# Optimization experiments

Hardware: AMD Instinct MI355X
Metric: run time of the kernel (lower is better)

Reference implementation:

```python
import jax, jax.numpy as jnp
import numpy as np

N_NODES = 50000
N_EDGES = 800000
IN_CH, HID_CH, OUT_CH = 128, 128, 40


def _glorot(key, fan_in, fan_out):
    lim = jnp.sqrt(6.0 / (fan_in + fan_out))
    return jax.random.uniform(key, (fan_in, fan_out), jnp.float32, -lim, lim)


def setup_inputs() -> dict:
    key = jax.random.key(0)
    ks = jax.random.split(key, 5)
    x = jax.random.normal(ks[0], (N_NODES, IN_CH), jnp.float32)
    edge_index = jax.random.randint(ks[1], (2, N_EDGES), 0, N_NODES, dtype=jnp.int32)
    return {
        "x": x,
        "edge_index": edge_index,
        "W1": _glorot(ks[2], IN_CH, HID_CH),
        "b1": jnp.zeros((HID_CH,), jnp.float32),
        "W2": _glorot(ks[3], HID_CH, HID_CH),
        "b2": jnp.zeros((HID_CH,), jnp.float32),
        "W3": _glorot(ks[4], HID_CH, OUT_CH),
        "b3": jnp.zeros((OUT_CH,), jnp.float32),
    }


def reference(x, edge_index, W1, b1, W2, b2, W3, b3):
    # Dropout is inference-mode identity (training=False). GCNConv (PyG default):
    # add self-loops, symmetric normalization D^-1/2 A_hat D^-1/2, linear + bias.
    n = x.shape[0]
    loop = jnp.arange(n, dtype=edge_index.dtype)
    src = jnp.concatenate([edge_index[0], loop])  # message sources
    dst = jnp.concatenate([edge_index[1], loop])  # aggregation targets
    deg = jax.ops.segment_sum(jnp.ones_like(src, dtype=x.dtype), dst, num_segments=n)
    dinv = jnp.where(deg > 0, deg ** -0.5, 0.0)
    norm = dinv[src] * dinv[dst]  # [E+N], identical across layers

    def conv(h, W, b):
        h = h @ W                                   # [N, F_out]
        msg = h[src] * norm[:, None]                # gather + scale: [E+N, F_out]
        return jax.ops.segment_sum(msg, dst, num_segments=n) + b

    h = jax.nn.relu(conv(x, W1, b1))
    h = jax.nn.relu(conv(h, W2, b2))
    h = conv(h, W3, b3)
    return jax.nn.log_softmax(h, axis=1)
```

## Files before the change

kernel.cpp:

```cpp
#include <hip/hip_runtime.h>
#include <math.h>


typedef short s8v __attribute__((ext_vector_type(8)));
typedef float f4v __attribute__((ext_vector_type(4)));
typedef unsigned short u16;

#define CSR_CAP 64

__device__ inline unsigned short f2b(float f) {
  unsigned int u = __float_as_uint(f);
  return (unsigned short)((u + 0x7fffu + ((u >> 16) & 1u)) >> 16);
}
__device__ inline float b2f(unsigned short b) {
  return __uint_as_float(((unsigned int)b) << 16);
}
__device__ inline f4v mfma16(s8v a, s8v b, f4v c) {
  return __builtin_amdgcn_mfma_f32_16x16x32_bf16(a, b, c, 0, 0, 0);
}

__device__ inline void pack_w_elem(const float* __restrict__ W,
                                   short* __restrict__ Wp, int FOUT_real,
                                   int NCT, int idx) {
  const int j = idx & 7;
  const int lane = (idx >> 3) & 63;
  const int fct = idx >> 9;
  const int ks = fct / NCT, ct = fct - ks * NCT;
  const int k = ks * 32 + (lane >> 4) * 8 + j;
  const int c = ct * 16 + (lane & 15);
  const float v = (c < FOUT_real) ? W[k * FOUT_real + c] : 0.f;
  Wp[idx] = (short)f2b(v);
}

__global__ __launch_bounds__(256) void k_soup(
    const float* __restrict__ x, const float* __restrict__ W1,
    short* __restrict__ Tb1, int nRowTiles, int gemmNB,
    const int* __restrict__ src, const int* __restrict__ dst,
    int* __restrict__ cnt, u16* __restrict__ col, int e, float inv8n,
    int fillNB, const float* __restrict__ W2, short* __restrict__ Wp2,
    const float* __restrict__ W3, short* __restrict__ Wp3) {
  __shared__ short Ws[4 * 8 * 64 * 8];
  const int bid = blockIdx.x;
  const int tid = threadIdx.x;

  if (bid < gemmNB) {
    const float4* w4 = (const float4*)W1;
    for (int it = 0; it < 16; ++it) {
      const int lin4 = it * 256 + tid;
      const int k = lin4 >> 5;
      const float4 v = w4[lin4];
      const int cb = (lin4 & 31) * 4;
      const int ks = k >> 5, kr = k & 31;
      const int laneBase = (kr >> 3) << 4;
      const int j = kr & 7;
      const float fv[4] = {v.x, v.y, v.z, v.w};
#pragma unroll
      for (int q = 0; q < 4; ++q) {
        const int c = cb + q;
        Ws[((ks * 8 + (c >> 4)) * 64 + (laneBase | (c & 15))) * 8 + j] =
            (short)f2b(fv[q]);
      }
    }
    __syncthreads();
    const int wid = tid >> 6, lane = tid & 63;
    const int rowTile = bid * 4 + wid;
    if (rowTile >= nRowTiles) return;
    const int row0 = rowTile * 16;
    const int arow = row0 + (lane & 15);
    const int kcol = (lane >> 4) * 8;
    f4v acc[8];
#pragma unroll
    for (int ct = 0; ct < 8; ++ct) acc[ct] = (f4v)(0.f);
    const float* ap = x + (size_t)arow * 128 + kcol;
#pragma unroll
    for (int ks = 0; ks < 4; ++ks) {
      const float4 a0 = *(const float4*)(ap + ks * 32);
      const float4 a1 = *(const float4*)(ap + ks * 32 + 4);
      s8v af;
      af[0] = (short)f2b(a0.x); af[1] = (short)f2b(a0.y);
      af[2] = (short)f2b(a0.z); af[3] = (short)f2b(a0.w);
      af[4] = (short)f2b(a1.x); af[5] = (short)f2b(a1.y);
      af[6] = (short)f2b(a1.z); af[7] = (short)f2b(a1.w);
#pragma unroll
      for (int ct = 0; ct < 8; ++ct) {
        const s8v bf = *(const s8v*)(Ws + ((ks * 8 + ct) * 64 + lane) * 8);
        acc[ct] = mfma16(af, bf, acc[ct]);
      }
    }
    const int crow0 = row0 + (lane >> 4) * 4;
    const int ccol = lane & 15;
#pragma unroll
    for (int r = 0; r < 4; ++r) {
      short* orow = Tb1 + (size_t)(crow0 + r) * 128 + ccol;
#pragma unroll
      for (int ct = 0; ct < 8; ++ct) orow[ct * 16] = (short)f2b(acc[ct][r]);
    }
  } else if (bid < gemmNB + fillNB) {
    const int fb = bid - gemmNB;
    const int bin = fb & 7;
    const int scanB = fb >> 3;
    const int stride = (fillNB >> 3) * 256;
    for (int i = scanB * 256 + tid; i < e; i += stride) {
      const int d = dst[i];
      int b = (int)((float)d * inv8n);
      b = b > 7 ? 7 : b;
      if (b == bin) {
        const int idx = atomicAdd(&cnt[d], 1);
        __builtin_nontemporal_store((u16)src[i], &col[(size_t)d * CSR_CAP + idx]);
      }
    }
  } else {
    int pb = bid - gemmNB - fillNB;
    if (pb < 64) {
      pack_w_elem(W2, Wp2, 128, 8, pb * 256 + tid);
    } else {
      const int idx = (pb - 64) * 256 + tid;
      if (idx < 128 * 48) pack_w_elem(W3, Wp3, 40, 3, idx);
    }
  }
}

__global__ __launch_bounds__(256) void k_dinvf(const int* __restrict__ cnt,
                                               float* __restrict__ dnf,
                                               int n, int rows_pad) {
  int i = blockIdx.x * 256 + threadIdx.x;
  if (i < rows_pad) dnf[i] = (i < n) ? rsqrtf((float)(cnt[i] + 1)) : 0.f;
}

template <int FOUT, bool PRESCALED>
__global__ __launch_bounds__(256) void k_aggemm(const short* __restrict__ Tb,
                                                const int* __restrict__ cnt,
                                                const u16* __restrict__ col,
                                                const float* __restrict__ dnf,
                                                const float* __restrict__ bias,
                                                const short* __restrict__ Wp,
                                                short* __restrict__ Tout, int n) {
  __shared__ short Ht[32 * 128];
  const int tid = threadIdx.x;
  const int base = blockIdx.x * 32;

#pragma unroll
  for (int pass = 0; pass < 2; ++pass) {
    const int nl = pass * 16 + (tid >> 4);
    const int node = base + nl;
    const int c8 = tid & 15;
    const int c0 = c8 * 8;
    float r[8];
#pragma unroll
    for (int j = 0; j < 8; ++j) r[j] = 0.f;
    if (node < n) {
      const int cn = cnt[node];
      const float dn = dnf[node];
      float acc[8];
      {
        const s8v v = *(const s8v*)(Tb + (size_t)node * 128 + c0);
#pragma unroll
        for (int j = 0; j < 8; ++j)
          acc[j] = (PRESCALED ? 1.f : dn) * b2f((unsigned short)v[j]);
      }
      const u16* cp = col + (size_t)node * CSR_CAP;
      int k = 0;
      for (; k + 4 <= cn; k += 4) {
        const int s0 = cp[k], s1 = cp[k + 1], s2 = cp[k + 2], s3 = cp[k + 3];
        const s8v v0 = *(const s8v*)(Tb + (size_t)s0 * 128 + c0);
        const s8v v1 = *(const s8v*)(Tb + (size_t)s1 * 128 + c0);
        const s8v v2 = *(const s8v*)(Tb + (size_t)s2 * 128 + c0);
        const s8v v3 = *(const s8v*)(Tb + (size_t)s3 * 128 + c0);
        if (PRESCALED) {
#pragma unroll
          for (int j = 0; j < 8; ++j)
            acc[j] += b2f((unsigned short)v0[j]) + b2f((unsigned short)v1[j]) +
                      b2f((unsigned short)v2[j]) + b2f((unsigned short)v3[j]);
        } else {
          const float d0 = dnf[s0], d1 = dnf[s1], d2 = dnf[s2], d3 = dnf[s3];
#pragma unroll
          for (int j = 0; j < 8; ++j)
            acc[j] += d0 * b2f((unsigned short)v0[j]) +
                      d1 * b2f((unsigned short)v1[j]) +
                      d2 * b2f((unsigned short)v2[j]) +
                      d3 * b2f((unsigned short)v3[j]);
        }
      }
      for (; k < cn; ++k) {
        const int s = cp[k];
        const s8v v = *(const s8v*)(Tb + (size_t)s * 128 + c0);
        const float ds = PRESCALED ? 1.f : dnf[s];
#pragma unroll
        for (int j = 0; j < 8; ++j) acc[j] += ds * b2f((unsigned short)v[j]);
      }
#pragma unroll
      for (int j = 0; j < 8; ++j)
        r[j] = fmaxf(acc[j] * dn + bias[c0 + j], 0.f);
    }
    s8v o;
#pragma unroll
    for (int j = 0; j < 8; ++j) o[j] = (short)f2b(r[j]);
    *(s8v*)((char*)Ht + nl * 256 + ((c0 * 2) ^ ((nl & 7) << 4))) = o;
  }
  __syncthreads();

  constexpr int NCT = FOUT / 16;
  const int wid = tid >> 6, lane = tid & 63;
  const int tile = wid >> 1;
  int ct0, nct;
  if (FOUT == 128) { ct0 = (wid & 1) * 4; nct = 4; }
  else { ct0 = 0; nct = (wid & 1) ? 0 : NCT; }
  if (nct > 0) {
    f4v acc[4];
#pragma unroll
    for (int j = 0; j < 4; ++j) acc[j] = (f4v)(0.f);
    const int lrow = tile * 16 + (lane & 15);
    const int kbase = (lane >> 4) * 8;
#pragma unroll
    for (int ks = 0; ks < 4; ++ks) {
      const int kcol = kbase + ks * 32;
      const s8v af = *(const s8v*)((const char*)Ht + lrow * 256 +
                                   ((kcol * 2) ^ ((lrow & 7) << 4)));
#pragma unroll
      for (int j = 0; j < 4; ++j) {
        if (j < nct) {
          const s8v bf =
              *(const s8v*)(Wp + ((ks * NCT + ct0 + j) * 64 + lane) * 8);
          acc[j] = mfma16(af, bf, acc[j]);
        }
      }
    }
    const int crow0 = base + tile * 16 + (lane >> 4) * 4;
    const int ccol = lane & 15;
#pragma unroll
    for (int r = 0; r < 4; ++r) {
      const float sc = dnf[crow0 + r];
      short* orow = Tout + (size_t)(crow0 + r) * FOUT + ccol;
#pragma unroll
      for (int j = 0; j < 4; ++j)
        if (j < nct) orow[(ct0 + j) * 16] = (short)f2b(acc[j][r] * sc);
    }
  }
}

__global__ __launch_bounds__(256) void k_agg3_lsm(const short* __restrict__ Tb,
                                                  const int* __restrict__ cnt,
                                                  const u16* __restrict__ col,
                                                  const float* __restrict__ dnf,
                                                  const float* __restrict__ bias,
                                                  float* __restrict__ out, int n) {
  const int gtid = blockIdx.x * 256 + threadIdx.x;
  const int node = gtid >> 3;
  const int c8 = gtid & 7;
  if (node >= n) return;
  const int c0 = c8 * 8;
  const bool valid = c8 < 5;
  const int cn = cnt[node];
  const float dn = dnf[node];
  float acc[8];
#pragma unroll
  for (int j = 0; j < 8; ++j) acc[j] = 0.f;
  const u16* cp = col + (size_t)node * CSR_CAP;
  if (valid) {
    const s8v v = *(const s8v*)(Tb + (size_t)node * 48 + c0);
#pragma unroll
    for (int j = 0; j < 8; ++j) acc[j] = b2f((unsigned short)v[j]);
    int k = 0;
    for (; k + 4 <= cn; k += 4) {
      const int s0 = cp[k], s1 = cp[k + 1], s2 = cp[k + 2], s3 = cp[k + 3];
      const s8v v0 = *(const s8v*)(Tb + (size_t)s0 * 48 + c0);
      const s8v v1 = *(const s8v*)(Tb + (size_t)s1 * 48 + c0);
      const s8v v2 = *(const s8v*)(Tb + (size_t)s2 * 48 + c0);
      const s8v v3 = *(const s8v*)(Tb + (size_t)s3 * 48 + c0);
#pragma unroll
      for (int j = 0; j < 8; ++j)
        acc[j] += b2f((unsigned short)v0[j]) + b2f((unsigned short)v1[j]) +
                  b2f((unsigned short)v2[j]) + b2f((unsigned short)v3[j]);
    }
    for (; k < cn; ++k) {
      const int s = cp[k];
      const s8v v = *(const s8v*)(Tb + (size_t)s * 48 + c0);
#pragma unroll
      for (int j = 0; j < 8; ++j) acc[j] += b2f((unsigned short)v[j]);
    }
  }
  float r[8];
  float m = -INFINITY;
#pragma unroll
  for (int j = 0; j < 8; ++j) {
    r[j] = valid ? (acc[j] * dn + bias[c0 + j]) : -INFINITY;
    m = fmaxf(m, r[j]);
  }
#pragma unroll
  for (int w = 1; w < 8; w <<= 1) m = fmaxf(m, __shfl_xor(m, w, 64));
  float s = 0.f;
#pragma unroll
  for (int j = 0; j < 8; ++j) s += expf(r[j] - m);
#pragma unroll
  for (int w = 1; w < 8; w <<= 1) s += __shfl_xor(s, w, 64);
  const float ls = logf(s);
  if (valid) {
    float* op = out + (size_t)node * 40 + c0;
    *(float4*)op = make_float4(r[0] - m - ls, r[1] - m - ls, r[2] - m - ls,
                               r[3] - m - ls);
    *(float4*)(op + 4) = make_float4(r[4] - m - ls, r[5] - m - ls,
                                     r[6] - m - ls, r[7] - m - ls);
  }
}

extern "C" void kernel_launch(void* const* d_in, const int* in_sizes, int n_in,
                              void* d_out, int out_size, void* d_ws,
                              size_t ws_size, hipStream_t stream) {
  const float* x  = (const float*)d_in[0];
  const int*   ei = (const int*)d_in[1];
  const float* W1 = (const float*)d_in[2];
  const float* b1 = (const float*)d_in[3];
  const float* W2 = (const float*)d_in[4];
  const float* b2 = (const float*)d_in[5];
  const float* W3 = (const float*)d_in[6];
  const float* b3 = (const float*)d_in[7];
  float* out = (float*)d_out;

  const int n = in_sizes[0] / 128;
  const int e = in_sizes[1] / 2;
  const int* src = ei;
  const int* dst = ei + e;

  char* ws = (char*)d_ws;
  size_t off = 0;
  auto carve = [&](size_t bytes) -> void* {
    void* p = ws + off;
    off = (off + bytes + 255) & ~(size_t)255;
    return p;
  };
  const int nb32 = (n + 31) / 32;
  const int rows_pad = nb32 * 32;

  int*   cnt = (int*)carve((size_t)n * 4);
  float* dnf = (float*)carve((size_t)rows_pad * 4);
  u16*   col = (u16*)carve((size_t)n * CSR_CAP * 2);
  short* A   = (short*)carve((size_t)rows_pad * 128 * 2);
  short* B   = (short*)carve((size_t)rows_pad * 128 * 2);
  short* Wp2 = (short*)carve(128 * 128 * 2);
  short* Wp3 = (short*)carve(128 * 48 * 2);

  const int nRowTiles = (n + 15) / 16;
  const int gemmNB = (nRowTiles + 3) / 4;
  const int fillNB = 2048;
  const int soupNB = gemmNB + fillNB + 64 + 24;

  hipMemsetAsync(cnt, 0, (size_t)n * 4, stream);
  k_soup<<<soupNB, 256, 0, stream>>>(x, W1, B, nRowTiles, gemmNB, src, dst,
                                     cnt, col, e, 8.0f / (float)n, fillNB,
                                     W2, Wp2, W3, Wp3);
  k_dinvf<<<(rows_pad + 255) / 256, 256, 0, stream>>>(cnt, dnf, n, rows_pad);
  k_aggemm<128, false><<<nb32, 256, 0, stream>>>(B, cnt, col, dnf, b1, Wp2, A, n);
  k_aggemm<48, true><<<nb32, 256, 0, stream>>>(A, cnt, col, dnf, b2, Wp3, B, n);
  k_agg3_lsm<<<((size_t)n * 8 + 255) / 256, 256, 0, stream>>>(B, cnt, col, dnf,
                                                              b3, out, n);
}
```

Baseline: 221.9 us.

## Fold degree normalization into consumers and shrink layer-3 feature stride to 40

The separate k_dinvf kernel and its dnf buffer are removed. Each consumer now computes rsqrt(cnt+1) inline from the degree counts, which drops one launch and the dnf array traffic at the cost of extra rsqrt work per gathered neighbour. The layer-3 intermediate is stored with a 40-column row stride instead of 48, with the stores masked, so each row is smaller to gather. The nontemporal store used in CSR fill becomes a plain store.

```diff
diff --git a/kernel.cpp b/kernel.cpp
--- a/kernel.cpp
+++ b/kernel.cpp
@@ -106,7 +106,7 @@
       b = b > 7 ? 7 : b;
       if (b == bin) {
         const int idx = atomicAdd(&cnt[d], 1);
-        __builtin_nontemporal_store((u16)src[i], &col[(size_t)d * CSR_CAP + idx]);
+        col[(size_t)d * CSR_CAP + idx] = (u16)src[i];
       }
     }
   } else {
@@ -120,18 +120,10 @@
   }
 }
 
-__global__ __launch_bounds__(256) void k_dinvf(const int* __restrict__ cnt,
-                                               float* __restrict__ dnf,
-                                               int n, int rows_pad) {
-  int i = blockIdx.x * 256 + threadIdx.x;
-  if (i < rows_pad) dnf[i] = (i < n) ? rsqrtf((float)(cnt[i] + 1)) : 0.f;
-}
-
 template <int FOUT, bool PRESCALED>
 __global__ __launch_bounds__(256) void k_aggemm(const short* __restrict__ Tb,
                                                 const int* __restrict__ cnt,
                                                 const u16* __restrict__ col,
-                                                const float* __restrict__ dnf,
                                                 const float* __restrict__ bias,
                                                 const short* __restrict__ Wp,
                                                 short* __restrict__ Tout, int n) {
@@ -150,7 +142,7 @@
     for (int j = 0; j < 8; ++j) r[j] = 0.f;
     if (node < n) {
       const int cn = cnt[node];
-      const float dn = dnf[node];
+      const float dn = rsqrtf((float)(cn + 1));
       float acc[8];
       {
         const s8v v = *(const s8v*)(Tb + (size_t)node * 128 + c0);
@@ -172,7 +164,10 @@
             acc[j] += b2f((unsigned short)v0[j]) + b2f((unsigned short)v1[j]) +
                       b2f((unsigned short)v2[j]) + b2f((unsigned short)v3[j]);
         } else {
-          const float d0 = dnf[s0], d1 = dnf[s1], d2 = dnf[s2], d3 = dnf[s3];
+          const float d0 = rsqrtf((float)(cnt[s0] + 1));
+          const float d1 = rsqrtf((float)(cnt[s1] + 1));
+          const float d2 = rsqrtf((float)(cnt[s2] + 1));
+          const float d3 = rsqrtf((float)(cnt[s3] + 1));
 #pragma unroll
           for (int j = 0; j < 8; ++j)
             acc[j] += d0 * b2f((unsigned short)v0[j]) +
@@ -184,7 +179,7 @@
       for (; k < cn; ++k) {
         const int s = cp[k];
         const s8v v = *(const s8v*)(Tb + (size_t)s * 128 + c0);
-        const float ds = PRESCALED ? 1.f : dnf[s];
+        const float ds = PRESCALED ? 1.f : rsqrtf((float)(cnt[s] + 1));
 #pragma unroll
         for (int j = 0; j < 8; ++j) acc[j] += ds * b2f((unsigned short)v[j]);
       }
@@ -199,7 +194,7 @@
   }
   __syncthreads();
 
-  constexpr int NCT = FOUT / 16;
+  constexpr int NCT = (FOUT == 128) ? 8 : 3;
   const int wid = tid >> 6, lane = tid & 63;
   const int tile = wid >> 1;
   int ct0, nct;
@@ -229,11 +224,17 @@
     const int ccol = lane & 15;
 #pragma unroll
     for (int r = 0; r < 4; ++r) {
-      const float sc = dnf[crow0 + r];
-      short* orow = Tout + (size_t)(crow0 + r) * FOUT + ccol;
-#pragma unroll
-      for (int j = 0; j < 4; ++j)
-        if (j < nct) orow[(ct0 + j) * 16] = (short)f2b(acc[j][r] * sc);
+      const int row = crow0 + r;
+      const float sc = (row < n) ? rsqrtf((float)(cnt[row] + 1)) : 0.f;
+      short* orow = Tout + (size_t)row * FOUT + ccol;
+#pragma unroll
+      for (int j = 0; j < 4; ++j) {
+        if (j < nct) {
+          const int c = (ct0 + j) * 16 + ccol;
+          if (FOUT == 128 || c < 40)
+            orow[(ct0 + j) * 16] = (short)f2b(acc[j][r] * sc);
+        }
+      }
     }
   }
 }
@@ -241,7 +242,6 @@
 __global__ __launch_bounds__(256) void k_agg3_lsm(const short* __restrict__ Tb,
                                                   const int* __restrict__ cnt,
                                                   const u16* __restrict__ col,
-                                                  const float* __restrict__ dnf,
                                                   const float* __restrict__ bias,
                                                   float* __restrict__ out, int n) {
   const int gtid = blockIdx.x * 256 + threadIdx.x;
@@ -251,22 +251,22 @@
   const int c0 = c8 * 8;
   const bool valid = c8 < 5;
   const int cn = cnt[node];
-  const float dn = dnf[node];
+  const float dn = rsqrtf((float)(cn + 1));
   float acc[8];
 #pragma unroll
   for (int j = 0; j < 8; ++j) acc[j] = 0.f;
   const u16* cp = col + (size_t)node * CSR_CAP;
   if (valid) {
-    const s8v v = *(const s8v*)(Tb + (size_t)node * 48 + c0);
+    const s8v v = *(const s8v*)(Tb + (size_t)node * 40 + c0);
 #pragma unroll
     for (int j = 0; j < 8; ++j) acc[j] = b2f((unsigned short)v[j]);
     int k = 0;
     for (; k + 4 <= cn; k += 4) {
       const int s0 = cp[k], s1 = cp[k + 1], s2 = cp[k + 2], s3 = cp[k + 3];
-      const s8v v0 = *(const s8v*)(Tb + (size_t)s0 * 48 + c0);
-      const s8v v1 = *(const s8v*)(Tb + (size_t)s1 * 48 + c0);
-      const s8v v2 = *(const s8v*)(Tb + (size_t)s2 * 48 + c0);
-      const s8v v3 = *(const s8v*)(Tb + (size_t)s3 * 48 + c0);
+      const s8v v0 = *(const s8v*)(Tb + (size_t)s0 * 40 + c0);
+      const s8v v1 = *(const s8v*)(Tb + (size_t)s1 * 40 + c0);
+      const s8v v2 = *(const s8v*)(Tb + (size_t)s2 * 40 + c0);
+      const s8v v3 = *(const s8v*)(Tb + (size_t)s3 * 40 + c0);
 #pragma unroll
       for (int j = 0; j < 8; ++j)
         acc[j] += b2f((unsigned short)v0[j]) + b2f((unsigned short)v1[j]) +
@@ -274,7 +274,7 @@
     }
     for (; k < cn; ++k) {
       const int s = cp[k];
-      const s8v v = *(const s8v*)(Tb + (size_t)s * 48 + c0);
+      const s8v v = *(const s8v*)(Tb + (size_t)s * 40 + c0);
 #pragma unroll
       for (int j = 0; j < 8; ++j) acc[j] += b2f((unsigned short)v[j]);
     }
@@ -290,7 +290,7 @@
   for (int w = 1; w < 8; w <<= 1) m = fmaxf(m, __shfl_xor(m, w, 64));
   float s = 0.f;
 #pragma unroll
-  for (int j = 0; j < 8; ++j) s += expf(r[j] - m);
+  for (int j = 0; j < 8; ++j) s += valid ? expf(r[j] - m) : 0.f;
 #pragma unroll
   for (int w = 1; w < 8; w <<= 1) s += __shfl_xor(s, w, 64);
   const float ls = logf(s);
@@ -332,7 +332,6 @@
   const int rows_pad = nb32 * 32;
 
   int*   cnt = (int*)carve((size_t)n * 4);
-  float* dnf = (float*)carve((size_t)rows_pad * 4);
   u16*   col = (u16*)carve((size_t)n * CSR_CAP * 2);
   short* A   = (short*)carve((size_t)rows_pad * 128 * 2);
   short* B   = (short*)carve((size_t)rows_pad * 128 * 2);
@@ -348,9 +347,8 @@
   k_soup<<<soupNB, 256, 0, stream>>>(x, W1, B, nRowTiles, gemmNB, src, dst,
                                      cnt, col, e, 8.0f / (float)n, fillNB,
                                      W2, Wp2, W3, Wp3);
-  k_dinvf<<<(rows_pad + 255) / 256, 256, 0, stream>>>(cnt, dnf, n, rows_pad);
-  k_aggemm<128, false><<<nb32, 256, 0, stream>>>(B, cnt, col, dnf, b1, Wp2, A, n);
-  k_aggemm<48, true><<<nb32, 256, 0, stream>>>(A, cnt, col, dnf, b2, Wp3, B, n);
-  k_agg3_lsm<<<((size_t)n * 8 + 255) / 256, 256, 0, stream>>>(B, cnt, col, dnf,
-                                                              b3, out, n);
-}
+  k_aggemm<128, false><<<nb32, 256, 0, stream>>>(B, cnt, col, b1, Wp2, A, n);
+  k_aggemm<40, true><<<nb32, 256, 0, stream>>>(A, cnt, col, b2, Wp3, B, n);
+  k_agg3_lsm<<<((size_t)n * 8 + 255) / 256, 256, 0, stream>>>(B, cnt, col, b3,
+                                                              out, n);
+}
```

Result: no change. 218.2 us (-1.6%).
